# Optimization experiments

Measured on AMD Instinct MI355X. Metric: run time of the kernel, lower is better.

## Reference

```python
import jax, jax.numpy as jnp
import numpy as np

B, T, C, D = 16, 4096, 1024, 64  # batch, tokens, d_model, head dim (d_model // n_heads)


def setup_inputs() -> dict:
    key = jax.random.key(0)
    kx, kq, kk, kv = jax.random.split(key, 4)
    scale_w = 1.0 / np.sqrt(C)
    return {
        "x": jax.random.normal(kx, (B, T, C), dtype=jnp.float32),
        "Wq": jax.random.normal(kq, (C, D), dtype=jnp.float32) * scale_w,
        "Wk": jax.random.normal(kk, (C, D), dtype=jnp.float32) * scale_w,
        "Wv": jax.random.normal(kv, (C, D), dtype=jnp.float32) * scale_w,
    }


def reference(x, Wq, Wk, Wv):
    # q, k, v: [B, T, D]; bias-free linear projections
    q = jnp.einsum("btc,cd->btd", x, Wq)
    k = jnp.einsum("btc,cd->btd", x, Wk)
    v = jnp.einsum("btc,cd->btd", x, Wv)
    # scores scaled by C**-0.5 (full d_model, matching the original module)
    scale = jnp.asarray(C, x.dtype) ** -0.5
    wei = jnp.einsum("bqd,bkd->bqk", q, k) * scale  # [B, T, T]
    wei = jax.nn.softmax(wei, axis=-1)
    # dropout is identity in eval mode
    return jnp.einsum("bqk,bkd->bqd", wei, v)  # [B, T, D]
```

## Files before the change

kernel.cpp:

```cpp
#include <hip/hip_runtime.h>
#include <stdint.h>

#define B_ 16
#define T_ 4096
#define C_ 1024
#define D_ 64
#define LOG2E 1.4426950408889634f

using f32x4 = __attribute__((ext_vector_type(4))) float;
using f32x16 = __attribute__((ext_vector_type(16))) float;
using bf16x8 = __attribute__((ext_vector_type(8))) short;
union U8 { uint32_t u[4]; bf16x8 v; };

__device__ __forceinline__ unsigned short f2bf(float x) {
  union { float f; uint32_t u; } v; v.f = x;
  uint32_t r = (v.u + 0x7fffu + ((v.u >> 16) & 1u)) >> 16;
  return (unsigned short)r;
}

__device__ __forceinline__ uint32_t cvtpk(float lo, float hi) {
  uint32_t r;
  asm("v_cvt_pk_bf16_f32 %0, %1, %2" : "=v"(r) : "v"(lo), "v"(hi));
  return r;
}

__device__ __forceinline__ void plswap(uint32_t& a, uint32_t& b) {
  asm volatile("v_permlane32_swap_b32 %0, %1" : "+v"(a), "+v"(b));
}

__device__ __forceinline__ void gload16(const void* gptr, void* lptr) {
  auto g = (const __attribute__((address_space(1))) uint32_t*)(uintptr_t)gptr;
  auto l = (__attribute__((address_space(3))) uint32_t*)(uintptr_t)lptr;
  __builtin_amdgcn_global_load_lds(g, l, 16, 0, 0);
}

#define SYNC_VM0()      asm volatile("s_waitcnt vmcnt(0)\ns_barrier" ::: "memory")
#define SYNC_VM0_LGKM() asm volatile("s_waitcnt vmcnt(0) lgkmcnt(0)\ns_barrier" ::: "memory")
#define SYNC_LGKM()     asm volatile("s_waitcnt lgkmcnt(0)\ns_barrier" ::: "memory")

__global__ void k_prep(const float* __restrict__ Wq, const float* __restrict__ Wk,
                       const float* __restrict__ Wv, unsigned short* __restrict__ Wt) {
  int idx = blockIdx.x * 256 + threadIdx.x;
  int n = idx >> 10, k = idx & 1023;
  const float* W = (n < 64) ? Wq : (n < 128 ? Wk : Wv);
  Wt[idx] = f2bf(W[(size_t)k * 64 + (n & 63)]);
}

__global__ __launch_bounds__(256) void k_proj(const float* __restrict__ X,
                                              const unsigned short* __restrict__ Wt,
                                              unsigned short* __restrict__ Qo,
                                              unsigned short* __restrict__ Ko,
                                              unsigned short* __restrict__ Vto) {
  __shared__ float Xs[128 * 32];
  __shared__ unsigned short Ws[192 * 32];
  const int tid = threadIdx.x;
  const int wave = tid >> 6, lane = tid & 63;
  const int g = lane >> 4, c = lane & 15;
  const int m0 = blockIdx.x * 128;

  f32x4 acc[2][12];
#pragma unroll
  for (int a = 0; a < 2; ++a)
#pragma unroll
    for (int b2 = 0; b2 < 12; ++b2) acc[a][b2] = f32x4{0.f, 0.f, 0.f, 0.f};

  const int xrow = tid >> 3, xseg = tid & 7;
  const int wrow = tid >> 2, wseg = tid & 3;

  for (int step = 0; step < 32; ++step) {
    const int k0 = step * 32;
#pragma unroll
    for (int p = 0; p < 4; ++p) {
      int row = p * 32 + xrow;
      int seg = xseg ^ (row & 7);
      gload16(X + (size_t)(m0 + row) * C_ + k0 + seg * 4,
              (char*)Xs + p * 4096 + wave * 1024);
    }
#pragma unroll
    for (int p = 0; p < 3; ++p) {
      int n = p * 64 + wrow;
      int seg = wseg ^ ((n >> 1) & 3);
      gload16(Wt + (size_t)n * C_ + k0 + seg * 8,
              (char*)Ws + p * 4096 + wave * 1024);
    }
    __syncthreads();

    bf16x8 af[2];
#pragma unroll
    for (int mi = 0; mi < 2; ++mi) {
      int row = wave * 32 + mi * 16 + c;
      int sub = g * 2;
      f32x4 x0 = *(const f32x4*)((const char*)Xs + row * 128 + (((sub) ^ (row & 7)) * 16));
      f32x4 x1 = *(const f32x4*)((const char*)Xs + row * 128 + (((sub + 1) ^ (row & 7)) * 16));
      bf16x8 t;
      t[0] = (short)f2bf(x0[0]); t[1] = (short)f2bf(x0[1]);
      t[2] = (short)f2bf(x0[2]); t[3] = (short)f2bf(x0[3]);
      t[4] = (short)f2bf(x1[0]); t[5] = (short)f2bf(x1[1]);
      t[6] = (short)f2bf(x1[2]); t[7] = (short)f2bf(x1[3]);
      af[mi] = t;
    }
#pragma unroll
    for (int ni = 0; ni < 12; ++ni) {
      int n = ni * 16 + c;
      bf16x8 bf = *(const bf16x8*)((const char*)Ws + n * 64 + ((g ^ ((n >> 1) & 3)) * 16));
      acc[0][ni] = __builtin_amdgcn_mfma_f32_16x16x32_bf16(af[0], bf, acc[0][ni], 0, 0, 0);
      acc[1][ni] = __builtin_amdgcn_mfma_f32_16x16x32_bf16(af[1], bf, acc[1][ni], 0, 0, 0);
    }
    __syncthreads();
  }

  const int b = m0 >> 12;
#pragma unroll
  for (int mi = 0; mi < 2; ++mi) {
    int r0 = m0 + wave * 32 + mi * 16 + g * 4;
#pragma unroll
    for (int ni = 0; ni < 12; ++ni) {
      int col = ni * 16 + c;
      if (ni < 4) {
#pragma unroll
        for (int i = 0; i < 4; ++i)
          Qo[(size_t)(r0 + i) * D_ + col] = f2bf(acc[mi][ni][i] * (0.03125f * LOG2E));
      } else if (ni < 8) {
        int d = col - 64;
#pragma unroll
        for (int i = 0; i < 4; ++i)
          Ko[(size_t)(r0 + i) * D_ + d] = f2bf(acc[mi][ni][i]);
      } else {
        int d = col - 128;
        int tt = r0 & (T_ - 1);
        ushort4 pk;
        pk.x = f2bf(acc[mi][ni][0]); pk.y = f2bf(acc[mi][ni][1]);
        pk.z = f2bf(acc[mi][ni][2]); pk.w = f2bf(acc[mi][ni][3]);
        *(ushort4*)(Vto + (size_t)b * (D_ * T_) + (size_t)d * T_ + tt) = pk;
      }
    }
  }
}

__global__ __launch_bounds__(256, 2) void k_attn(const unsigned short* __restrict__ Qi,
                                                 const unsigned short* __restrict__ Ki,
                                                 const unsigned short* __restrict__ Vti,
                                                 float* __restrict__ Out) {
  __shared__ char LDSBUF[6 * 8192];

  const int tid = threadIdx.x;
  const int wave = tid >> 6, lane = tid & 63;
  const int ql = lane & 31;
  const int hi = lane >> 5;
  const int qsel = wave & 1;
  const int th = wave >> 1;
  const int b = blockIdx.y;
  const int qb = blockIdx.x * 128 + qsel * 64;

  const unsigned short* Qb = Qi + (size_t)b * T_ * D_;
  const unsigned short* Kb = Ki + (size_t)b * T_ * D_;
  const unsigned short* Vb = Vti + (size_t)b * D_ * T_;

  bf16x8 qf[2][4];
#pragma unroll
  for (int qg = 0; qg < 2; ++qg)
#pragma unroll
    for (int ks = 0; ks < 4; ++ks)
      qf[qg][ks] = *(const bf16x8*)(Qb + (size_t)(qb + qg * 32 + ql) * D_ + ks * 16 + 8 * hi);

  f32x16 o00, o01, o10, o11;
  float l_loc0 = 0.f, l_loc1 = 0.f;
#pragma unroll
  for (int i = 0; i < 16; ++i) { o00[i] = 0.f; o01[i] = 0.f; o10[i] = 0.f; o11[i] = 0.f; }

  const int srow = tid >> 3, sseg = tid & 7;

#define STAGE(BUF, KT)                                                          \
  do {                                                                          \
    char* kb_ = LDSBUF + (BUF) * 8192 + wave * 1024;                            \
    char* vb_ = LDSBUF + 24576 + (BUF) * 8192 + wave * 1024;                    \
    _Pragma("unroll") for (int p = 0; p < 2; ++p) {                             \
      int row = p * 32 + srow;                                                  \
      int seg = sseg ^ (row & 7);                                               \
      gload16(Kb + (size_t)((KT) * 64 + row) * D_ + seg * 8, kb_ + p * 4096);   \
      gload16(Vb + (size_t)row * T_ + (KT) * 64 + seg * 8, vb_ + p * 4096);     \
    }                                                                           \
  } while (0)

#define PACK_TB(SC, LREF, PB0, PB1)                                             \
  do {                                                                          \
    float p_[16];                                                               \
    _Pragma("unroll") for (int r = 0; r < 16; ++r)                              \
        p_[r] = __builtin_amdgcn_exp2f((SC)[r]);                                \
    float a0 = (p_[0] + p_[1]) + (p_[2] + p_[3]);                               \
    float a1 = (p_[4] + p_[5]) + (p_[6] + p_[7]);                               \
    float a2 = (p_[8] + p_[9]) + (p_[10] + p_[11]);                             \
    float a3 = (p_[12] + p_[13]) + (p_[14] + p_[15]);                           \
    LREF += (a0 + a1) + (a2 + a3);                                              \
    uint32_t w00 = cvtpk(p_[0], p_[1]),   w01 = cvtpk(p_[2], p_[3]);            \
    uint32_t w10 = cvtpk(p_[4], p_[5]),   w11 = cvtpk(p_[6], p_[7]);            \
    uint32_t w20 = cvtpk(p_[8], p_[9]),   w21 = cvtpk(p_[10], p_[11]);          \
    uint32_t w30 = cvtpk(p_[12], p_[13]), w31 = cvtpk(p_[14], p_[15]);          \
    plswap(w00, w10); plswap(w01, w11);                                         \
    plswap(w20, w30); plswap(w21, w31);                                         \
    { U8 t_; t_.u[0] = w00; t_.u[1] = w01; t_.u[2] = w10; t_.u[3] = w11;        \
      PB0 = t_.v; }                                                             \
    { U8 t_; t_.u[0] = w20; t_.u[1] = w21; t_.u[2] = w30; t_.u[3] = w31;        \
      PB1 = t_.v; }                                                             \
  } while (0)

#define TILE_COMPUTE(BUF)                                                       \
  do {                                                                          \
    const char* kb_ = LDSBUF + (BUF) * 8192;                                    \
    const char* vb_ = LDSBUF + 24576 + (BUF) * 8192;                            \
    f32x16 s0, s1;                                                              \
    _Pragma("unroll") for (int i = 0; i < 16; ++i) { s0[i] = 0.f; s1[i] = 0.f; }\
    __builtin_amdgcn_s_setprio(1);                                              \
    _Pragma("unroll") for (int ks = 0; ks < 4; ++ks) {                          \
      int sg = ((2 * ks + hi) ^ (ql & 7)) * 16;                                 \
      bf16x8 kf = *(const bf16x8*)(kb_ + (th * 32 + ql) * 128 + sg);            \
      s0 = __builtin_amdgcn_mfma_f32_32x32x16_bf16(kf, qf[0][ks], s0, 0, 0, 0); \
      s1 = __builtin_amdgcn_mfma_f32_32x32x16_bf16(kf, qf[1][ks], s1, 0, 0, 0); \
    }                                                                           \
    __builtin_amdgcn_s_setprio(0);                                              \
    bf16x8 pb00, pb01, pb10, pb11;                                              \
    PACK_TB(s0, l_loc0, pb00, pb01);                                            \
    PACK_TB(s1, l_loc1, pb10, pb11);                                            \
    __builtin_amdgcn_s_setprio(1);                                              \
    _Pragma("unroll") for (int ts = 0; ts < 2; ++ts) {                          \
      bf16x8 pb0_ = ts ? pb01 : pb00;                                           \
      bf16x8 pb1_ = ts ? pb11 : pb10;                                           \
      int sgv = ((4 * th + 2 * ts + hi) ^ (ql & 7)) * 16;                       \
      bf16x8 vf0 = *(const bf16x8*)(vb_ + ql * 128 + sgv);                      \
      bf16x8 vf1 = *(const bf16x8*)(vb_ + (32 + ql) * 128 + sgv);               \
      o00 = __builtin_amdgcn_mfma_f32_32x32x16_bf16(vf0, pb0_, o00, 0, 0, 0);   \
      o10 = __builtin_amdgcn_mfma_f32_32x32x16_bf16(vf0, pb1_, o10, 0, 0, 0);   \
      o01 = __builtin_amdgcn_mfma_f32_32x32x16_bf16(vf1, pb0_, o01, 0, 0, 0);   \
      o11 = __builtin_amdgcn_mfma_f32_32x32x16_bf16(vf1, pb1_, o11, 0, 0, 0);   \
    }                                                                           \
    __builtin_amdgcn_s_setprio(0);                                              \
  } while (0)

  STAGE(0, 0);
  STAGE(1, 1);
  int cur = 0;
  for (int kt = 0; kt < 62; ++kt) {
    SYNC_VM0();
    int nxt = cur + 2; if (nxt >= 3) nxt -= 3;
    STAGE(nxt, kt + 2);
    TILE_COMPUTE(cur);
    ++cur; if (cur == 3) cur = 0;
  }
  SYNC_VM0();
  TILE_COMPUTE(cur);
  SYNC_VM0();
  TILE_COMPUTE(0);

  float l0 = l_loc0 + __shfl_xor(l_loc0, 32);
  float l1 = l_loc1 + __shfl_xor(l_loc1, 32);

  SYNC_VM0_LGKM();
  if (wave >= 2) {
    char* mo = LDSBUF + qsel * 20480 + lane * 256;
#pragma unroll
    for (int rq = 0; rq < 4; ++rq) {
      *(f32x4*)(mo + rq * 16)       = f32x4{o00[4*rq], o00[4*rq+1], o00[4*rq+2], o00[4*rq+3]};
      *(f32x4*)(mo + 64 + rq * 16)  = f32x4{o01[4*rq], o01[4*rq+1], o01[4*rq+2], o01[4*rq+3]};
      *(f32x4*)(mo + 128 + rq * 16) = f32x4{o10[4*rq], o10[4*rq+1], o10[4*rq+2], o10[4*rq+3]};
      *(f32x4*)(mo + 192 + rq * 16) = f32x4{o11[4*rq], o11[4*rq+1], o11[4*rq+2], o11[4*rq+3]};
    }
    *(float*)(LDSBUF + 44032 + qsel * 512 + lane * 8)     = l0;
    *(float*)(LDSBUF + 44032 + qsel * 512 + lane * 8 + 4) = l1;
  }
  SYNC_LGKM();
  if (wave < 2) {
    const char* mo = LDSBUF + qsel * 20480 + lane * 256;
    float lp0 = *(const float*)(LDSBUF + 44032 + qsel * 512 + lane * 8);
    float lp1 = *(const float*)(LDSBUF + 44032 + qsel * 512 + lane * 8 + 4);
    float inv0 = 1.0f / (l0 + lp0);
    float inv1 = 1.0f / (l1 + lp1);
    float* Ob0 = Out + ((size_t)b * T_ + qb + ql) * D_;
    float* Ob1 = Out + ((size_t)b * T_ + qb + 32 + ql) * D_;
#pragma unroll
    for (int rq = 0; rq < 4; ++rq) {
      f32x4 p0 = *(const f32x4*)(mo + rq * 16);
      f32x4 p1 = *(const f32x4*)(mo + 64 + rq * 16);
      f32x4 p2 = *(const f32x4*)(mo + 128 + rq * 16);
      f32x4 p3 = *(const f32x4*)(mo + 192 + rq * 16);
      f32x4 t0, t1, t2, t3;
#pragma unroll
      for (int i = 0; i < 4; ++i) {
        t0[i] = (o00[4*rq+i] + p0[i]) * inv0;
        t1[i] = (o01[4*rq+i] + p1[i]) * inv0;
        t2[i] = (o10[4*rq+i] + p2[i]) * inv1;
        t3[i] = (o11[4*rq+i] + p3[i]) * inv1;
      }
      *(f32x4*)(Ob0 + rq * 8 + hi * 4)      = t0;
      *(f32x4*)(Ob0 + 32 + rq * 8 + hi * 4) = t1;
      *(f32x4*)(Ob1 + rq * 8 + hi * 4)      = t2;
      *(f32x4*)(Ob1 + 32 + rq * 8 + hi * 4) = t3;
    }
  }
#undef STAGE
#undef PACK_TB
#undef TILE_COMPUTE
}

extern "C" void kernel_launch(void* const* d_in, const int* in_sizes, int n_in,
                              void* d_out, int out_size, void* d_ws, size_t ws_size,
                              hipStream_t stream) {
  const float* x  = (const float*)d_in[0];
  const float* Wq = (const float*)d_in[1];
  const float* Wk = (const float*)d_in[2];
  const float* Wv = (const float*)d_in[3];
  float* out = (float*)d_out;
  char* ws = (char*)d_ws;
  unsigned short* Wt = (unsigned short*)(ws);
  unsigned short* Qb = (unsigned short*)(ws + (1u << 20));
  unsigned short* Kb = (unsigned short*)(ws + (9u << 20));
  unsigned short* Vt = (unsigned short*)(ws + (17u << 20));

  k_prep<<<768, 256, 0, stream>>>(Wq, Wk, Wv, Wt);
  k_proj<<<512, 256, 0, stream>>>(x, Wt, Qb, Kb, Vt);
  k_attn<<<dim3(T_ / 128, B_), 256, 0, stream>>>(Qb, Kb, Vt, out);
}
```

Baseline: 154.1 us.

## Give each wave private double-buffered K/V LDS slices and drop block barriers

Each wave now stages only the K rows and V columns it consumes (its th half) into a private double-buffered LDS region, replacing the shared triple buffer. Per-tile block-wide s_barrier is removed and replaced with a per-wave vmcnt(8) wait, so waves no longer synchronize with each other in the main loop. The cost is that the two waves sharing a th half both load the same data (duplicate global traffic), LDS grows to 64 KB per block, which may limit occupancy at two blocks per CU, and prefetch depth drops from two tiles to one.

```diff
diff --git a/kernel.cpp b/kernel.cpp
--- a/kernel.cpp
+++ b/kernel.cpp
@@ -34,9 +34,13 @@
   __builtin_amdgcn_global_load_lds(g, l, 16, 0, 0);
 }
 
-#define SYNC_VM0()      asm volatile("s_waitcnt vmcnt(0)\ns_barrier" ::: "memory")
 #define SYNC_VM0_LGKM() asm volatile("s_waitcnt vmcnt(0) lgkmcnt(0)\ns_barrier" ::: "memory")
 #define SYNC_LGKM()     asm volatile("s_waitcnt lgkmcnt(0)\ns_barrier" ::: "memory")
+
+#define WAIT8() do { asm volatile("s_waitcnt vmcnt(8)" ::: "memory"); \
+                     __builtin_amdgcn_sched_barrier(0); } while (0)
+#define WAIT0() do { asm volatile("s_waitcnt vmcnt(0)" ::: "memory"); \
+                     __builtin_amdgcn_sched_barrier(0); } while (0)
 
 __global__ void k_prep(const float* __restrict__ Wq, const float* __restrict__ Wk,
                        const float* __restrict__ Wv, unsigned short* __restrict__ Wt) {
@@ -141,7 +145,7 @@
                                                  const unsigned short* __restrict__ Ki,
                                                  const unsigned short* __restrict__ Vti,
                                                  float* __restrict__ Out) {
-  __shared__ char LDSBUF[6 * 8192];
+  __shared__ char LDSBUF[4 * 16384];
 
   const int tid = threadIdx.x;
   const int wave = tid >> 6, lane = tid & 63;
@@ -155,6 +159,7 @@
   const unsigned short* Qb = Qi + (size_t)b * T_ * D_;
   const unsigned short* Kb = Ki + (size_t)b * T_ * D_;
   const unsigned short* Vb = Vti + (size_t)b * D_ * T_;
+  char* LDSW = LDSBUF + wave * 16384;
 
   bf16x8 qf[2][4];
 #pragma unroll
@@ -168,18 +173,19 @@
 #pragma unroll
   for (int i = 0; i < 16; ++i) { o00[i] = 0.f; o01[i] = 0.f; o10[i] = 0.f; o11[i] = 0.f; }
 
-  const int srow = tid >> 3, sseg = tid & 7;
+  const int krow = lane >> 3, kswz = (lane & 7) ^ (krow & 7);
+  const int vrow = lane >> 2, vswz = (lane & 3) ^ ((vrow >> 1) & 3);
 
 #define STAGE(BUF, KT)                                                          \
   do {                                                                          \
-    char* kb_ = LDSBUF + (BUF) * 8192 + wave * 1024;                            \
-    char* vb_ = LDSBUF + 24576 + (BUF) * 8192 + wave * 1024;                    \
-    _Pragma("unroll") for (int p = 0; p < 2; ++p) {                             \
-      int row = p * 32 + srow;                                                  \
-      int seg = sseg ^ (row & 7);                                               \
-      gload16(Kb + (size_t)((KT) * 64 + row) * D_ + seg * 8, kb_ + p * 4096);   \
-      gload16(Vb + (size_t)row * T_ + (KT) * 64 + seg * 8, vb_ + p * 4096);     \
-    }                                                                           \
+    char* kb_ = LDSW + (BUF) * 8192;                                            \
+    char* vb_ = kb_ + 4096;                                                     \
+    _Pragma("unroll") for (int p = 0; p < 4; ++p)                               \
+      gload16(Kb + (size_t)((KT) * 64 + th * 32 + p * 8 + krow) * 64 + kswz * 8,\
+              kb_ + p * 1024);                                                  \
+    _Pragma("unroll") for (int p = 0; p < 4; ++p)                               \
+      gload16(Vb + (size_t)(p * 16 + vrow) * T_ + (KT) * 64 + th * 32 + vswz * 8,\
+              vb_ + p * 1024);                                                  \
   } while (0)
 
 #define PACK_TB(SC, LREF, PB0, PB1)                                             \
@@ -206,14 +212,14 @@
 
 #define TILE_COMPUTE(BUF)                                                       \
   do {                                                                          \
-    const char* kb_ = LDSBUF + (BUF) * 8192;                                    \
-    const char* vb_ = LDSBUF + 24576 + (BUF) * 8192;                            \
+    const char* kb_ = LDSW + (BUF) * 8192;                                      \
+    const char* vb_ = kb_ + 4096;                                               \
     f32x16 s0, s1;                                                              \
     _Pragma("unroll") for (int i = 0; i < 16; ++i) { s0[i] = 0.f; s1[i] = 0.f; }\
     __builtin_amdgcn_s_setprio(1);                                              \
     _Pragma("unroll") for (int ks = 0; ks < 4; ++ks) {                          \
       int sg = ((2 * ks + hi) ^ (ql & 7)) * 16;                                 \
-      bf16x8 kf = *(const bf16x8*)(kb_ + (th * 32 + ql) * 128 + sg);            \
+      bf16x8 kf = *(const bf16x8*)(kb_ + ql * 128 + sg);                        \
       s0 = __builtin_amdgcn_mfma_f32_32x32x16_bf16(kf, qf[0][ks], s0, 0, 0, 0); \
       s1 = __builtin_amdgcn_mfma_f32_32x32x16_bf16(kf, qf[1][ks], s1, 0, 0, 0); \
     }                                                                           \
@@ -225,9 +231,9 @@
     _Pragma("unroll") for (int ts = 0; ts < 2; ++ts) {                          \
       bf16x8 pb0_ = ts ? pb01 : pb00;                                           \
       bf16x8 pb1_ = ts ? pb11 : pb10;                                           \
-      int sgv = ((4 * th + 2 * ts + hi) ^ (ql & 7)) * 16;                       \
-      bf16x8 vf0 = *(const bf16x8*)(vb_ + ql * 128 + sgv);                      \
-      bf16x8 vf1 = *(const bf16x8*)(vb_ + (32 + ql) * 128 + sgv);               \
+      int sgv = ((2 * ts + hi) ^ ((ql >> 1) & 3)) * 16;                         \
+      bf16x8 vf0 = *(const bf16x8*)(vb_ + ql * 64 + sgv);                       \
+      bf16x8 vf1 = *(const bf16x8*)(vb_ + (32 + ql) * 64 + sgv);                \
       o00 = __builtin_amdgcn_mfma_f32_32x32x16_bf16(vf0, pb0_, o00, 0, 0, 0);   \
       o10 = __builtin_amdgcn_mfma_f32_32x32x16_bf16(vf0, pb1_, o10, 0, 0, 0);   \
       o01 = __builtin_amdgcn_mfma_f32_32x32x16_bf16(vf1, pb0_, o01, 0, 0, 0);   \
@@ -237,19 +243,15 @@
   } while (0)
 
   STAGE(0, 0);
-  STAGE(1, 1);
   int cur = 0;
-  for (int kt = 0; kt < 62; ++kt) {
-    SYNC_VM0();
-    int nxt = cur + 2; if (nxt >= 3) nxt -= 3;
-    STAGE(nxt, kt + 2);
+  for (int kt = 0; kt < 63; ++kt) {
+    STAGE(cur ^ 1, kt + 1);
+    WAIT8();
     TILE_COMPUTE(cur);
-    ++cur; if (cur == 3) cur = 0;
-  }
-  SYNC_VM0();
+    cur ^= 1;
+  }
+  WAIT0();
   TILE_COMPUTE(cur);
-  SYNC_VM0();
-  TILE_COMPUTE(0);
 
   float l0 = l_loc0 + __shfl_xor(l_loc0, 32);
   float l1 = l_loc1 + __shfl_xor(l_loc1, 32);
```

Measured after the change: 163.3 us. +6.0%, slower.

## Load K/V fragments directly from global into registers, dropping LDS staging

Applied to the files above, without the earlier changes.

Replaces the triple-buffered global_load_lds staging of K and Vt tiles, and its per-tile barriers, with direct per-wave global loads into register fragments, double-buffered in registers. LDS is now used only for the final merge of partial outputs, which shrinks shared memory and removes all barriers from the main loop. In exchange, each K/V element is read from global or L2 by both query-half waves instead of once per block. The extra register buffers could also hurt occupancy or latency hiding.

```diff
diff --git a/kernel.cpp b/kernel.cpp
--- a/kernel.cpp
+++ b/kernel.cpp
@@ -33,10 +33,6 @@
   auto l = (__attribute__((address_space(3))) uint32_t*)(uintptr_t)lptr;
   __builtin_amdgcn_global_load_lds(g, l, 16, 0, 0);
 }
-
-#define SYNC_VM0()      asm volatile("s_waitcnt vmcnt(0)\ns_barrier" ::: "memory")
-#define SYNC_VM0_LGKM() asm volatile("s_waitcnt vmcnt(0) lgkmcnt(0)\ns_barrier" ::: "memory")
-#define SYNC_LGKM()     asm volatile("s_waitcnt lgkmcnt(0)\ns_barrier" ::: "memory")
 
 __global__ void k_prep(const float* __restrict__ Wq, const float* __restrict__ Wk,
                        const float* __restrict__ Wv, unsigned short* __restrict__ Wt) {
@@ -141,7 +137,7 @@
                                                  const unsigned short* __restrict__ Ki,
                                                  const unsigned short* __restrict__ Vti,
                                                  float* __restrict__ Out) {
-  __shared__ char LDSBUF[6 * 8192];
+  __shared__ char MERGE[34816];
 
   const int tid = threadIdx.x;
   const int wave = tid >> 6, lane = tid & 63;
@@ -153,8 +149,8 @@
   const int qb = blockIdx.x * 128 + qsel * 64;
 
   const unsigned short* Qb = Qi + (size_t)b * T_ * D_;
-  const unsigned short* Kb = Ki + (size_t)b * T_ * D_;
-  const unsigned short* Vb = Vti + (size_t)b * D_ * T_;
+  const unsigned short* Kp = Ki + (size_t)b * T_ * D_ + (size_t)(th * 32 + ql) * D_ + hi * 8;
+  const unsigned short* Vp = Vti + (size_t)b * D_ * T_ + (size_t)ql * T_ + th * 32 + hi * 8;
 
   bf16x8 qf[2][4];
 #pragma unroll
@@ -168,17 +164,14 @@
 #pragma unroll
   for (int i = 0; i < 16; ++i) { o00[i] = 0.f; o01[i] = 0.f; o10[i] = 0.f; o11[i] = 0.f; }
 
-  const int srow = tid >> 3, sseg = tid & 7;
-
-#define STAGE(BUF, KT)                                                          \
+#define LOADT(KT, KF, VF)                                                       \
   do {                                                                          \
-    char* kb_ = LDSBUF + (BUF) * 8192 + wave * 1024;                            \
-    char* vb_ = LDSBUF + 24576 + (BUF) * 8192 + wave * 1024;                    \
-    _Pragma("unroll") for (int p = 0; p < 2; ++p) {                             \
-      int row = p * 32 + srow;                                                  \
-      int seg = sseg ^ (row & 7);                                               \
-      gload16(Kb + (size_t)((KT) * 64 + row) * D_ + seg * 8, kb_ + p * 4096);   \
-      gload16(Vb + (size_t)row * T_ + (KT) * 64 + seg * 8, vb_ + p * 4096);     \
+    _Pragma("unroll") for (int ks = 0; ks < 4; ++ks)                            \
+      KF[ks] = *(const bf16x8*)(Kp + (size_t)(KT) * (64 * D_) + ks * 16);       \
+    _Pragma("unroll") for (int tv = 0; tv < 4; ++tv) {                          \
+      int ts_ = tv >> 1, db_ = tv & 1;                                          \
+      VF[tv] = *(const bf16x8*)(Vp + (size_t)db_ * (32 * T_) +                  \
+                                (size_t)(KT) * 64 + ts_ * 16);                  \
     }                                                                           \
   } while (0)
 
@@ -204,59 +197,48 @@
       PB1 = t_.v; }                                                             \
   } while (0)
 
-#define TILE_COMPUTE(BUF)                                                       \
+#define TILE_COMPUTE(KF, VF)                                                    \
   do {                                                                          \
-    const char* kb_ = LDSBUF + (BUF) * 8192;                                    \
-    const char* vb_ = LDSBUF + 24576 + (BUF) * 8192;                            \
     f32x16 s0, s1;                                                              \
     _Pragma("unroll") for (int i = 0; i < 16; ++i) { s0[i] = 0.f; s1[i] = 0.f; }\
     __builtin_amdgcn_s_setprio(1);                                              \
     _Pragma("unroll") for (int ks = 0; ks < 4; ++ks) {                          \
-      int sg = ((2 * ks + hi) ^ (ql & 7)) * 16;                                 \
-      bf16x8 kf = *(const bf16x8*)(kb_ + (th * 32 + ql) * 128 + sg);            \
-      s0 = __builtin_amdgcn_mfma_f32_32x32x16_bf16(kf, qf[0][ks], s0, 0, 0, 0); \
-      s1 = __builtin_amdgcn_mfma_f32_32x32x16_bf16(kf, qf[1][ks], s1, 0, 0, 0); \
+      s0 = __builtin_amdgcn_mfma_f32_32x32x16_bf16(KF[ks], qf[0][ks], s0, 0, 0, 0); \
+      s1 = __builtin_amdgcn_mfma_f32_32x32x16_bf16(KF[ks], qf[1][ks], s1, 0, 0, 0); \
     }                                                                           \
     __builtin_amdgcn_s_setprio(0);                                              \
     bf16x8 pb00, pb01, pb10, pb11;                                              \
     PACK_TB(s0, l_loc0, pb00, pb01);                                            \
     PACK_TB(s1, l_loc1, pb10, pb11);                                            \
     __builtin_amdgcn_s_setprio(1);                                              \
-    _Pragma("unroll") for (int ts = 0; ts < 2; ++ts) {                          \
-      bf16x8 pb0_ = ts ? pb01 : pb00;                                           \
-      bf16x8 pb1_ = ts ? pb11 : pb10;                                           \
-      int sgv = ((4 * th + 2 * ts + hi) ^ (ql & 7)) * 16;                       \
-      bf16x8 vf0 = *(const bf16x8*)(vb_ + ql * 128 + sgv);                      \
-      bf16x8 vf1 = *(const bf16x8*)(vb_ + (32 + ql) * 128 + sgv);               \
-      o00 = __builtin_amdgcn_mfma_f32_32x32x16_bf16(vf0, pb0_, o00, 0, 0, 0);   \
-      o10 = __builtin_amdgcn_mfma_f32_32x32x16_bf16(vf0, pb1_, o10, 0, 0, 0);   \
-      o01 = __builtin_amdgcn_mfma_f32_32x32x16_bf16(vf1, pb0_, o01, 0, 0, 0);   \
-      o11 = __builtin_amdgcn_mfma_f32_32x32x16_bf16(vf1, pb1_, o11, 0, 0, 0);   \
-    }                                                                           \
+    o00 = __builtin_amdgcn_mfma_f32_32x32x16_bf16(VF[0], pb00, o00, 0, 0, 0);   \
+    o10 = __builtin_amdgcn_mfma_f32_32x32x16_bf16(VF[0], pb10, o10, 0, 0, 0);   \
+    o01 = __builtin_amdgcn_mfma_f32_32x32x16_bf16(VF[1], pb00, o01, 0, 0, 0);   \
+    o11 = __builtin_amdgcn_mfma_f32_32x32x16_bf16(VF[1], pb10, o11, 0, 0, 0);   \
+    o00 = __builtin_amdgcn_mfma_f32_32x32x16_bf16(VF[2], pb01, o00, 0, 0, 0);   \
+    o10 = __builtin_amdgcn_mfma_f32_32x32x16_bf16(VF[2], pb11, o10, 0, 0, 0);   \
+    o01 = __builtin_amdgcn_mfma_f32_32x32x16_bf16(VF[3], pb01, o01, 0, 0, 0);   \
+    o11 = __builtin_amdgcn_mfma_f32_32x32x16_bf16(VF[3], pb11, o11, 0, 0, 0);   \
     __builtin_amdgcn_s_setprio(0);                                              \
   } while (0)
 
-  STAGE(0, 0);
-  STAGE(1, 1);
-  int cur = 0;
-  for (int kt = 0; kt < 62; ++kt) {
-    SYNC_VM0();
-    int nxt = cur + 2; if (nxt >= 3) nxt -= 3;
-    STAGE(nxt, kt + 2);
-    TILE_COMPUTE(cur);
-    ++cur; if (cur == 3) cur = 0;
-  }
-  SYNC_VM0();
-  TILE_COMPUTE(cur);
-  SYNC_VM0();
-  TILE_COMPUTE(0);
+  bf16x8 kA[4], vA[4], kB[4], vB[4];
+  LOADT(0, kA, vA);
+  for (int kt = 0; kt < 62; kt += 2) {
+    LOADT(kt + 1, kB, vB);
+    TILE_COMPUTE(kA, vA);
+    LOADT(kt + 2, kA, vA);
+    TILE_COMPUTE(kB, vB);
+  }
+  LOADT(63, kB, vB);
+  TILE_COMPUTE(kA, vA);
+  TILE_COMPUTE(kB, vB);
 
   float l0 = l_loc0 + __shfl_xor(l_loc0, 32);
   float l1 = l_loc1 + __shfl_xor(l_loc1, 32);
 
-  SYNC_VM0_LGKM();
   if (wave >= 2) {
-    char* mo = LDSBUF + qsel * 20480 + lane * 256;
+    char* mo = MERGE + qsel * 16384 + lane * 256;
 #pragma unroll
     for (int rq = 0; rq < 4; ++rq) {
       *(f32x4*)(mo + rq * 16)       = f32x4{o00[4*rq], o00[4*rq+1], o00[4*rq+2], o00[4*rq+3]};
@@ -264,14 +246,14 @@
       *(f32x4*)(mo + 128 + rq * 16) = f32x4{o10[4*rq], o10[4*rq+1], o10[4*rq+2], o10[4*rq+3]};
       *(f32x4*)(mo + 192 + rq * 16) = f32x4{o11[4*rq], o11[4*rq+1], o11[4*rq+2], o11[4*rq+3]};
     }
-    *(float*)(LDSBUF + 44032 + qsel * 512 + lane * 8)     = l0;
-    *(float*)(LDSBUF + 44032 + qsel * 512 + lane * 8 + 4) = l1;
-  }
-  SYNC_LGKM();
+    *(float*)(MERGE + 32768 + qsel * 512 + lane * 8)     = l0;
+    *(float*)(MERGE + 32768 + qsel * 512 + lane * 8 + 4) = l1;
+  }
+  __syncthreads();
   if (wave < 2) {
-    const char* mo = LDSBUF + qsel * 20480 + lane * 256;
-    float lp0 = *(const float*)(LDSBUF + 44032 + qsel * 512 + lane * 8);
-    float lp1 = *(const float*)(LDSBUF + 44032 + qsel * 512 + lane * 8 + 4);
+    const char* mo = MERGE + qsel * 16384 + lane * 256;
+    float lp0 = *(const float*)(MERGE + 32768 + qsel * 512 + lane * 8);
+    float lp1 = *(const float*)(MERGE + 32768 + qsel * 512 + lane * 8 + 4);
     float inv0 = 1.0f / (l0 + lp0);
     float inv1 = 1.0f / (l1 + lp1);
     float* Ob0 = Out + ((size_t)b * T_ + qb + ql) * D_;
@@ -296,7 +278,7 @@
       *(f32x4*)(Ob1 + 32 + rq * 8 + hi * 4) = t3;
     }
   }
-#undef STAGE
+#undef LOADT
 #undef PACK_TB
 #undef TILE_COMPUTE
 }
```

Result: slower. 198.1 us (+28.5%).
